# Optimization experiments

Measured on AMD Instinct MI355X. Metric: run time of the kernel, lower is better.

## Reference

```python
import jax, jax.numpy as jnp
import numpy as np

N, F_IN, F_HID, F_OUT = 16384, 128, 128, 64
EDGE_P = 0.001  # Bernoulli edge probability -> avg degree ~16


def _sage_conv(x, mask_t, deg_inv, Wl, b, Wr):
    # PyG SAGEConv (mean aggr): out = lin_l(mean_agg) + lin_r(x); lin_l has bias.
    agg = (mask_t @ x) * deg_inv[:, None]  # [N, Fin] mean over incoming edges
    return agg @ Wl.T + b + x @ Wr.T


def setup_inputs() -> dict:
    key = jax.random.key(0)
    ks = jax.random.split(key, 12)
    x = jax.random.normal(ks[0], (N, F_IN), dtype=jnp.float32)
    adj = (jax.random.uniform(ks[1], (N, N)) < EDGE_P).astype(jnp.float32)

    def lin(k, fo, fi):
        s = 1.0 / np.sqrt(fi)
        return jax.random.uniform(k, (fo, fi), jnp.float32, -s, s)

    dims = [(F_HID, F_IN), (F_HID, F_HID), (F_OUT, F_HID)]
    params = {}
    for i, (fo, fi) in enumerate(dims):
        params[f"Wl{i}"] = lin(ks[2 + 3 * i], fo, fi)
        params[f"b{i}"] = jnp.zeros((fo,), jnp.float32)
        params[f"Wr{i}"] = lin(ks[3 + 3 * i], fo, fi)
    return {"x": x, "adj": adj, **params}


def reference(x, adj, Wl0, b0, Wr0, Wl1, b1, Wr1, Wl2, b2, Wr2):
    # edge (r, c): adj[r, c] != 0, source r -> target c (PyG convention).
    mask = (adj != 0).astype(x.dtype)
    deg = mask.sum(axis=0)                      # incoming degree per target node
    deg_inv = jnp.where(deg > 0, 1.0 / jnp.maximum(deg, 1.0), 0.0)
    mask_t = mask.T                             # [target, source]
    # Dropout layers are identity in eval mode.
    h = jax.nn.relu(_sage_conv(x, mask_t, deg_inv, Wl0, b0, Wr0))
    h = jax.nn.relu(_sage_conv(h, mask_t, deg_inv, Wl1, b1, Wr1))
    out = _sage_conv(h, mask_t, deg_inv, Wl2, b2, Wr2)
    return out
```

## Files before the change

kernel.cpp:

```cpp
#include <hip/hip_runtime.h>


#define NN 16384
#define FIN 128
#define CAP (1 << 19)
#define LBUF 1024

typedef int iv4 __attribute__((ext_vector_type(4)));

#define OFF_CNT   0u
#define OFF_DEG   256u
#define OFF_OFFS  65792u
#define OFF_CUR   131584u
#define OFF_DINV  197120u
#define OFF_PAIRS 262656u
#define OFF_ESRC  (262656u + 8u * CAP)
#define OFF_WT0   (OFF_ESRC + 4u * CAP)
#define OFF_WT1   (OFF_WT0 + 131072u)
#define OFF_WT2   (OFF_WT1 + 131072u)
#define OFF_H1    (OFF_WT2 + 65536u)
#define OFF_H2    (OFF_H1 + 4u * NN * FIN)

__global__ void k_wt(const float* __restrict__ Wl0, const float* __restrict__ Wr0,
                     const float* __restrict__ Wl1, const float* __restrict__ Wr1,
                     const float* __restrict__ Wl2, const float* __restrict__ Wr2,
                     float* __restrict__ wt0, float* __restrict__ wt1,
                     float* __restrict__ wt2) {
    int g = blockIdx.x * 256 + threadIdx.x;
    if (g < 32768) {
        int k = g >> 7, o = g & 127;
        wt0[g] = (k < 128) ? Wl0[o * 128 + k] : Wr0[o * 128 + (k - 128)];
    } else if (g < 65536) {
        int gg = g - 32768;
        int k = gg >> 7, o = gg & 127;
        wt1[gg] = (k < 128) ? Wl1[o * 128 + k] : Wr1[o * 128 + (k - 128)];
    } else if (g < 81920) {
        int gg = g - 65536;
        int k = gg >> 6, o = gg & 63;
        wt2[gg] = (k < 128) ? Wl2[o * 128 + k] : Wr2[o * 128 + (k - 128)];
    }
}

__device__ __forceinline__ void emit_hits(iv4 v, int idx4, int* __restrict__ deg,
                                          unsigned int* lcnt,
                                          unsigned long long* lbuf) {
    if ((v.x | v.y | v.z | v.w) == 0) return;
    int base = idx4 << 2;
    int s = base >> 14;
    int t = base & (NN - 1);
    int w[4] = {v.x, v.y, v.z, v.w};
    #pragma unroll
    for (int k = 0; k < 4; ++k) {
        if (w[k] != 0) {
            atomicAdd(&deg[t + k], 1);
            unsigned int idx = atomicAdd(lcnt, 1u);
            if (idx < LBUF)
                lbuf[idx] = ((unsigned long long)s << 32) | (unsigned)(t + k);
        }
    }
}

__global__ __launch_bounds__(256) void k_count(
    const iv4* __restrict__ adj4, int* __restrict__ deg,
    unsigned int* __restrict__ cnt, unsigned long long* __restrict__ pairs) {
    __shared__ unsigned int lcnt;
    __shared__ unsigned int lbase;
    __shared__ unsigned long long lbuf[LBUF];
    const int tid = threadIdx.x;
    if (tid == 0) lcnt = 0;
    __syncthreads();

    const int stride = 2048 * 256;
    int i = blockIdx.x * 256 + tid;
    #pragma unroll 1
    for (int n = 0; n < 64; ++n, i += 2 * stride) {
        iv4 a = __builtin_nontemporal_load(&adj4[i]);
        iv4 b = __builtin_nontemporal_load(&adj4[i + stride]);
        emit_hits(a, i, deg, &lcnt, lbuf);
        emit_hits(b, i + stride, deg, &lcnt, lbuf);
    }
    __syncthreads();
    unsigned int total = lcnt;
    if (total > LBUF) total = LBUF;
    if (tid == 0) lbase = atomicAdd(cnt, total);
    __syncthreads();
    unsigned int bb = lbase;
    for (unsigned int j = tid; j < total; j += 256)
        if (bb + j < CAP) pairs[bb + j] = lbuf[j];
}

__global__ __launch_bounds__(1024) void k_scan(
    const int* __restrict__ deg, int* __restrict__ offs,
    int* __restrict__ cur, float* __restrict__ dinv) {
    __shared__ int ps[1024];
    int tid = threadIdx.x;
    int base = tid * 16;
    int local = 0;
    #pragma unroll
    for (int j = 0; j < 16; ++j) local += deg[base + j];
    ps[tid] = local;
    __syncthreads();
    for (int ofs = 1; ofs < 1024; ofs <<= 1) {
        int v = (tid >= ofs) ? ps[tid - ofs] : 0;
        __syncthreads();
        ps[tid] += v;
        __syncthreads();
    }
    int run = ps[tid] - local;
    #pragma unroll
    for (int j = 0; j < 16; ++j) {
        int d = deg[base + j];
        offs[base + j] = run;
        cur[base + j] = run;
        dinv[base + j] = d > 0 ? 1.0f / (float)d : 0.0f;
        run += d;
    }
    if (tid == 1023) offs[NN] = run;
}

__global__ void k_bin(const unsigned long long* __restrict__ pairs,
                      const unsigned int* __restrict__ cnt,
                      int* __restrict__ cur, int* __restrict__ esrc) {
    unsigned int total = *cnt;
    if (total > CAP) total = CAP;
    unsigned int stride = gridDim.x * blockDim.x;
    for (unsigned int i = blockIdx.x * blockDim.x + threadIdx.x; i < total; i += stride) {
        unsigned long long p = pairs[i];
        int s = (int)(p >> 32);
        int t = (int)(p & 0xFFFFFFFFull);
        int pos = atomicAdd(&cur[t], 1);
        esrc[pos] = s;
    }
}

template <int FOUT, bool RELU>
__global__ __launch_bounds__(256) void k_layer(
    const float4* __restrict__ hin,
    float* __restrict__ hout,
    const int* __restrict__ esrc, const int* __restrict__ offs,
    const float* __restrict__ dinv,
    const float4* __restrict__ Wt4,
    const float* __restrict__ bias)
{
    constexpr int S4 = 66;
    __shared__ float4 z[32 * S4];
    const int tid = threadIdx.x;
    const int nodeBase = blockIdx.x * 32;

    #pragma unroll
    for (int r = 0; r < 4; ++r) {
        int g = tid + 256 * r;
        int n = g >> 5, j = g & 31;
        z[n * S4 + 32 + j] = hin[(nodeBase + n) * 32 + j];
    }

    {
        const int nl = tid >> 3;
        const int q = tid & 7;
        const int node = nodeBase + nl;
        const int e0 = offs[node], e1 = offs[node + 1];
        float4 acc[4];
        #pragma unroll
        for (int k = 0; k < 4; ++k) acc[k] = make_float4(0.f, 0.f, 0.f, 0.f);
        int e = e0;
        for (; e + 2 <= e1; e += 2) {
            int s0 = esrc[e], s1 = esrc[e + 1];
            const float4* r0 = hin + s0 * 32;
            const float4* r1 = hin + s1 * 32;
            #pragma unroll
            for (int k = 0; k < 4; ++k) {
                float4 va = r0[q + 8 * k];
                float4 vb = r1[q + 8 * k];
                acc[k].x += va.x + vb.x; acc[k].y += va.y + vb.y;
                acc[k].z += va.z + vb.z; acc[k].w += va.w + vb.w;
            }
        }
        if (e < e1) {
            const float4* r0 = hin + esrc[e] * 32;
            #pragma unroll
            for (int k = 0; k < 4; ++k) {
                float4 va = r0[q + 8 * k];
                acc[k].x += va.x; acc[k].y += va.y;
                acc[k].z += va.z; acc[k].w += va.w;
            }
        }
        const float di = dinv[node];
        #pragma unroll
        for (int k = 0; k < 4; ++k) {
            acc[k].x *= di; acc[k].y *= di; acc[k].z *= di; acc[k].w *= di;
            z[nl * S4 + q + 8 * k] = acc[k];
        }
    }
    __syncthreads();

    constexpr int TO = FOUT / 4;
    constexpr int TN = 256 / TO;
    constexpr int NPT = 32 / TN;
    const int to = tid % TO;
    const int tn = tid / TO;

    float4 acc[NPT];
    #pragma unroll
    for (int m = 0; m < NPT; ++m) acc[m] = make_float4(0.f, 0.f, 0.f, 0.f);

    #pragma unroll 2
    for (int k4 = 0; k4 < 64; ++k4) {
        float4 w0 = Wt4[(4 * k4 + 0) * TO + to];
        float4 w1 = Wt4[(4 * k4 + 1) * TO + to];
        float4 w2 = Wt4[(4 * k4 + 2) * TO + to];
        float4 w3 = Wt4[(4 * k4 + 3) * TO + to];
        #pragma unroll
        for (int m = 0; m < NPT; ++m) {
            float4 a = z[(tn * NPT + m) * S4 + k4];
            acc[m].x += a.x * w0.x + a.y * w1.x + a.z * w2.x + a.w * w3.x;
            acc[m].y += a.x * w0.y + a.y * w1.y + a.z * w2.y + a.w * w3.y;
            acc[m].z += a.x * w0.z + a.y * w1.z + a.z * w2.z + a.w * w3.z;
            acc[m].w += a.x * w0.w + a.y * w1.w + a.z * w2.w + a.w * w3.w;
        }
    }

    const float4 bb = ((const float4*)bias)[to];
    #pragma unroll
    for (int m = 0; m < NPT; ++m) {
        float4 o;
        o.x = acc[m].x + bb.x; o.y = acc[m].y + bb.y;
        o.z = acc[m].z + bb.z; o.w = acc[m].w + bb.w;
        if (RELU) {
            o.x = fmaxf(o.x, 0.f); o.y = fmaxf(o.y, 0.f);
            o.z = fmaxf(o.z, 0.f); o.w = fmaxf(o.w, 0.f);
        }
        ((float4*)hout)[(nodeBase + tn * NPT + m) * TO + to] = o;
    }
}

extern "C" void kernel_launch(void* const* d_in, const int* in_sizes, int n_in,
                              void* d_out, int out_size, void* d_ws, size_t ws_size,
                              hipStream_t stream) {
    const float* x = (const float*)d_in[0];
    const iv4* adj4 = (const iv4*)d_in[1];
    const float* Wl0 = (const float*)d_in[2];
    const float* b0 = (const float*)d_in[3];
    const float* Wr0 = (const float*)d_in[4];
    const float* Wl1 = (const float*)d_in[5];
    const float* b1 = (const float*)d_in[6];
    const float* Wr1 = (const float*)d_in[7];
    const float* Wl2 = (const float*)d_in[8];
    const float* b2 = (const float*)d_in[9];
    const float* Wr2 = (const float*)d_in[10];

    char* ws = (char*)d_ws;
    unsigned int* cnt = (unsigned int*)(ws + OFF_CNT);
    int* deg = (int*)(ws + OFF_DEG);
    int* offs = (int*)(ws + OFF_OFFS);
    int* cur = (int*)(ws + OFF_CUR);
    float* dinv = (float*)(ws + OFF_DINV);
    unsigned long long* pairs = (unsigned long long*)(ws + OFF_PAIRS);
    int* esrc = (int*)(ws + OFF_ESRC);
    float* wt0 = (float*)(ws + OFF_WT0);
    float* wt1 = (float*)(ws + OFF_WT1);
    float* wt2 = (float*)(ws + OFF_WT2);
    float* h1 = (float*)(ws + OFF_H1);
    float* h2 = (float*)(ws + OFF_H2);

    (void)hipMemsetAsync(ws, 0, OFF_OFFS, stream);

    k_wt<<<320, 256, 0, stream>>>(Wl0, Wr0, Wl1, Wr1, Wl2, Wr2, wt0, wt1, wt2);
    k_count<<<2048, 256, 0, stream>>>(adj4, deg, cnt, pairs);
    k_scan<<<1, 1024, 0, stream>>>(deg, offs, cur, dinv);
    k_bin<<<512, 256, 0, stream>>>(pairs, cnt, cur, esrc);
    k_layer<128, true><<<NN / 32, 256, 0, stream>>>(
        (const float4*)x, h1, esrc, offs, dinv, (const float4*)wt0, b0);
    k_layer<128, true><<<NN / 32, 256, 0, stream>>>(
        (const float4*)h1, h2, esrc, offs, dinv, (const float4*)wt1, b1);
    k_layer<64, false><<<NN / 32, 256, 0, stream>>>(
        (const float4*)h2, (float*)d_out, esrc, offs, dinv, (const float4*)wt2, b2);
}
```

Before: 1.454 ms.

## Replace CSR build with fixed-capacity per-node neighbor slots filled during scan

Instead of collecting edge pairs, prefix-scanning degrees and binning into CSR, the adjacency scan now writes each source directly into a per-target slot array of fixed capacity 64, using the degree atomic as the slot index. This drops the scan and bin kernels, the pairs buffer, and the memset (degree zeroing moves into the weight-transpose kernel). It risks silently dropping neighbors for nodes with in-degree above 64 (the mean would then be wrong), and the neighbor order becomes nondeterministic. The 1024-entry per-block shared-memory pair buffer is also removed.

```diff
diff --git a/kernel.cpp b/kernel.cpp
--- a/kernel.cpp
+++ b/kernel.cpp
@@ -2,31 +2,25 @@
 
 
 #define NN 16384
-#define FIN 128
-#define CAP (1 << 19)
-#define LBUF 1024
+#define SLOTC 64
 
 typedef int iv4 __attribute__((ext_vector_type(4)));
 
-#define OFF_CNT   0u
-#define OFF_DEG   256u
-#define OFF_OFFS  65792u
-#define OFF_CUR   131584u
-#define OFF_DINV  197120u
-#define OFF_PAIRS 262656u
-#define OFF_ESRC  (262656u + 8u * CAP)
-#define OFF_WT0   (OFF_ESRC + 4u * CAP)
+#define OFF_DEG   0u
+#define OFF_SLOT  65536u
+#define OFF_WT0   (65536u + 4194304u)
 #define OFF_WT1   (OFF_WT0 + 131072u)
 #define OFF_WT2   (OFF_WT1 + 131072u)
 #define OFF_H1    (OFF_WT2 + 65536u)
-#define OFF_H2    (OFF_H1 + 4u * NN * FIN)
+#define OFF_H2    (OFF_H1 + 4u * NN * 128u)
 
 __global__ void k_wt(const float* __restrict__ Wl0, const float* __restrict__ Wr0,
                      const float* __restrict__ Wl1, const float* __restrict__ Wr1,
                      const float* __restrict__ Wl2, const float* __restrict__ Wr2,
                      float* __restrict__ wt0, float* __restrict__ wt1,
-                     float* __restrict__ wt2) {
+                     float* __restrict__ wt2, int* __restrict__ deg) {
     int g = blockIdx.x * 256 + threadIdx.x;
+    if (g < NN) deg[g] = 0;
     if (g < 32768) {
         int k = g >> 7, o = g & 127;
         wt0[g] = (k < 128) ? Wl0[o * 128 + k] : Wr0[o * 128 + (k - 128)];
@@ -42,8 +36,7 @@
 }
 
 __device__ __forceinline__ void emit_hits(iv4 v, int idx4, int* __restrict__ deg,
-                                          unsigned int* lcnt,
-                                          unsigned long long* lbuf) {
+                                          int* __restrict__ slots) {
     if ((v.x | v.y | v.z | v.w) == 0) return;
     int base = idx4 << 2;
     int s = base >> 14;
@@ -52,84 +45,23 @@
     #pragma unroll
     for (int k = 0; k < 4; ++k) {
         if (w[k] != 0) {
-            atomicAdd(&deg[t + k], 1);
-            unsigned int idx = atomicAdd(lcnt, 1u);
-            if (idx < LBUF)
-                lbuf[idx] = ((unsigned long long)s << 32) | (unsigned)(t + k);
+            int pos = atomicAdd(&deg[t + k], 1);
+            if (pos < SLOTC) slots[(t + k) * SLOTC + pos] = s;
         }
     }
 }
 
 __global__ __launch_bounds__(256) void k_count(
     const iv4* __restrict__ adj4, int* __restrict__ deg,
-    unsigned int* __restrict__ cnt, unsigned long long* __restrict__ pairs) {
-    __shared__ unsigned int lcnt;
-    __shared__ unsigned int lbase;
-    __shared__ unsigned long long lbuf[LBUF];
-    const int tid = threadIdx.x;
-    if (tid == 0) lcnt = 0;
-    __syncthreads();
-
+    int* __restrict__ slots) {
     const int stride = 2048 * 256;
-    int i = blockIdx.x * 256 + tid;
+    int i = blockIdx.x * 256 + threadIdx.x;
     #pragma unroll 1
     for (int n = 0; n < 64; ++n, i += 2 * stride) {
         iv4 a = __builtin_nontemporal_load(&adj4[i]);
         iv4 b = __builtin_nontemporal_load(&adj4[i + stride]);
-        emit_hits(a, i, deg, &lcnt, lbuf);
-        emit_hits(b, i + stride, deg, &lcnt, lbuf);
-    }
-    __syncthreads();
-    unsigned int total = lcnt;
-    if (total > LBUF) total = LBUF;
-    if (tid == 0) lbase = atomicAdd(cnt, total);
-    __syncthreads();
-    unsigned int bb = lbase;
-    for (unsigned int j = tid; j < total; j += 256)
-        if (bb + j < CAP) pairs[bb + j] = lbuf[j];
-}
-
-__global__ __launch_bounds__(1024) void k_scan(
-    const int* __restrict__ deg, int* __restrict__ offs,
-    int* __restrict__ cur, float* __restrict__ dinv) {
-    __shared__ int ps[1024];
-    int tid = threadIdx.x;
-    int base = tid * 16;
-    int local = 0;
-    #pragma unroll
-    for (int j = 0; j < 16; ++j) local += deg[base + j];
-    ps[tid] = local;
-    __syncthreads();
-    for (int ofs = 1; ofs < 1024; ofs <<= 1) {
-        int v = (tid >= ofs) ? ps[tid - ofs] : 0;
-        __syncthreads();
-        ps[tid] += v;
-        __syncthreads();
-    }
-    int run = ps[tid] - local;
-    #pragma unroll
-    for (int j = 0; j < 16; ++j) {
-        int d = deg[base + j];
-        offs[base + j] = run;
-        cur[base + j] = run;
-        dinv[base + j] = d > 0 ? 1.0f / (float)d : 0.0f;
-        run += d;
-    }
-    if (tid == 1023) offs[NN] = run;
-}
-
-__global__ void k_bin(const unsigned long long* __restrict__ pairs,
-                      const unsigned int* __restrict__ cnt,
-                      int* __restrict__ cur, int* __restrict__ esrc) {
-    unsigned int total = *cnt;
-    if (total > CAP) total = CAP;
-    unsigned int stride = gridDim.x * blockDim.x;
-    for (unsigned int i = blockIdx.x * blockDim.x + threadIdx.x; i < total; i += stride) {
-        unsigned long long p = pairs[i];
-        int s = (int)(p >> 32);
-        int t = (int)(p & 0xFFFFFFFFull);
-        int pos = atomicAdd(&cur[t], 1);
-        esrc[pos] = s;
+        emit_hits(a, i, deg, slots);
+        emit_hits(b, i + stride, deg, slots);
     }
 }
 
@@ -137,8 +69,7 @@
 __global__ __launch_bounds__(256) void k_layer(
     const float4* __restrict__ hin,
     float* __restrict__ hout,
-    const int* __restrict__ esrc, const int* __restrict__ offs,
-    const float* __restrict__ dinv,
+    const int* __restrict__ slots, const int* __restrict__ deg,
     const float4* __restrict__ Wt4,
     const float* __restrict__ bias)
 {
@@ -158,13 +89,15 @@
         const int nl = tid >> 3;
         const int q = tid & 7;
         const int node = nodeBase + nl;
-        const int e0 = offs[node], e1 = offs[node + 1];
+        const int d = deg[node];
+        const int dc = d < SLOTC ? d : SLOTC;
+        const int* el = slots + node * SLOTC;
         float4 acc[4];
         #pragma unroll
         for (int k = 0; k < 4; ++k) acc[k] = make_float4(0.f, 0.f, 0.f, 0.f);
-        int e = e0;
-        for (; e + 2 <= e1; e += 2) {
-            int s0 = esrc[e], s1 = esrc[e + 1];
+        int e = 0;
+        for (; e + 2 <= dc; e += 2) {
+            int s0 = el[e], s1 = el[e + 1];
             const float4* r0 = hin + s0 * 32;
             const float4* r1 = hin + s1 * 32;
             #pragma unroll
@@ -175,8 +108,8 @@
                 acc[k].z += va.z + vb.z; acc[k].w += va.w + vb.w;
             }
         }
-        if (e < e1) {
-            const float4* r0 = hin + esrc[e] * 32;
+        if (e < dc) {
+            const float4* r0 = hin + el[e] * 32;
             #pragma unroll
             for (int k = 0; k < 4; ++k) {
                 float4 va = r0[q + 8 * k];
@@ -184,7 +117,7 @@
                 acc[k].z += va.z; acc[k].w += va.w;
             }
         }
-        const float di = dinv[node];
+        const float di = d > 0 ? 1.0f / (float)d : 0.0f;
         #pragma unroll
         for (int k = 0; k < 4; ++k) {
             acc[k].x *= di; acc[k].y *= di; acc[k].z *= di; acc[k].w *= di;
@@ -249,29 +182,21 @@
     const float* Wr2 = (const float*)d_in[10];
 
     char* ws = (char*)d_ws;
-    unsigned int* cnt = (unsigned int*)(ws + OFF_CNT);
     int* deg = (int*)(ws + OFF_DEG);
-    int* offs = (int*)(ws + OFF_OFFS);
-    int* cur = (int*)(ws + OFF_CUR);
-    float* dinv = (float*)(ws + OFF_DINV);
-    unsigned long long* pairs = (unsigned long long*)(ws + OFF_PAIRS);
-    int* esrc = (int*)(ws + OFF_ESRC);
+    int* slots = (int*)(ws + OFF_SLOT);
     float* wt0 = (float*)(ws + OFF_WT0);
     float* wt1 = (float*)(ws + OFF_WT1);
     float* wt2 = (float*)(ws + OFF_WT2);
     float* h1 = (float*)(ws + OFF_H1);
     float* h2 = (float*)(ws + OFF_H2);
 
-    (void)hipMemsetAsync(ws, 0, OFF_OFFS, stream);
-
-    k_wt<<<320, 256, 0, stream>>>(Wl0, Wr0, Wl1, Wr1, Wl2, Wr2, wt0, wt1, wt2);
-    k_count<<<2048, 256, 0, stream>>>(adj4, deg, cnt, pairs);
-    k_scan<<<1, 1024, 0, stream>>>(deg, offs, cur, dinv);
-    k_bin<<<512, 256, 0, stream>>>(pairs, cnt, cur, esrc);
+    k_wt<<<320, 256, 0, stream>>>(Wl0, Wr0, Wl1, Wr1, Wl2, Wr2,
+                                  wt0, wt1, wt2, deg);
+    k_count<<<2048, 256, 0, stream>>>(adj4, deg, slots);
     k_layer<128, true><<<NN / 32, 256, 0, stream>>>(
-        (const float4*)x, h1, esrc, offs, dinv, (const float4*)wt0, b0);
+        (const float4*)x, h1, slots, deg, (const float4*)wt0, b0);
     k_layer<128, true><<<NN / 32, 256, 0, stream>>>(
-        (const float4*)h1, h2, esrc, offs, dinv, (const float4*)wt1, b1);
+        (const float4*)h1, h2, slots, deg, (const float4*)wt1, b1);
     k_layer<64, false><<<NN / 32, 256, 0, stream>>>(
-        (const float4*)h2, (float*)d_out, esrc, offs, dinv, (const float4*)wt2, b2);
-}
+        (const float4*)h2, (float*)d_out, slots, deg, (const float4*)wt2, b2);
+}
```

After: 1.436 ms. No clear change (-1.3%).
